# Kernel tuning notes

Hardware: AMD Instinct MI355X
Metric: run time of the kernel (lower is better)

Reference implementation:

```python
import jax, jax.numpy as jnp
import numpy as np

SAMPLE_RATE = 24000.0
HARMONIC_NUM = 8
SINE_AMP = 0.1
DIM = HARMONIC_NUM + 1
BATCH, LENGTH = 16, 480000


def setup_inputs() -> dict:
    key = jax.random.key(0)
    k1, k2, k3 = jax.random.split(key, 3)
    u = jax.random.uniform(k1, (BATCH, LENGTH), dtype=jnp.float32)
    voiced = (jax.random.uniform(k2, (BATCH, LENGTH)) > 0.2).astype(jnp.float32)
    f0 = (80.0 + 400.0 * u) * voiced
    rand_ini = jax.random.uniform(k3, (BATCH, 1, DIM), dtype=jnp.float32)
    return {"f0": f0, "rand_ini": rand_ini}


def reference(f0, rand_ini):
    # f0: [B, L] -> [B, L, 1]
    f0 = f0[..., None]
    harmonics = jnp.arange(1, DIM + 1, dtype=f0.dtype).reshape(1, 1, -1)  # [1,1,DIM]
    rad_values = jnp.mod(f0 * harmonics / SAMPLE_RATE, 1.0)              # [B,L,DIM]
    rad_values = rad_values.at[:, 0:1, :].add(rand_ini)                  # random initial phase
    phase = jnp.cumsum(rad_values, axis=1) * (2.0 * jnp.pi)              # [B,L,DIM]
    uv = (f0 > 0).astype(f0.dtype)                                       # [B,L,1]
    sine_waves = jnp.sin(phase) * SINE_AMP * uv                          # fused scale+mask
    return sine_waves, uv
```

## Files before the change

### kernel.cpp

```cpp
#include <hip/hip_runtime.h>
#include <math.h>

#define BATCH 16
#define LEN 480000
#define NDIM 9
#define CHUNK 4096
#define NCHUNK 118
#define AMP 0.1f

__device__ __forceinline__ float hw_fract(float x) {
#if __has_builtin(__builtin_amdgcn_fractf)
  return __builtin_amdgcn_fractf(x);
#else
  return x - floorf(x);
#endif
}
__device__ __forceinline__ float hw_sin1(float x) {
#if __has_builtin(__builtin_amdgcn_sinf)
  return __builtin_amdgcn_sinf(x);
#else
  return __sinf(x * 6.283185307179586f);
#endif
}

__global__ __launch_bounds__(256) void sg_partial(const float* __restrict__ f0,
                                                  double* __restrict__ part) {
  const int c = blockIdx.x, b = blockIdx.y, t = threadIdx.x;
  const float4* f4 = (const float4*)(f0 + (size_t)b * LEN);
  const int b4 = c * (CHUNK / 4);
  double s = 0.0;
#pragma unroll
  for (int p = 0; p < 4; ++p) {
    int i4 = b4 + p * 256 + t;
    if (i4 < LEN / 4) {
      float4 v = f4[i4];
      s += (double)((v.x + v.y) + (v.z + v.w));
    }
  }
#pragma unroll
  for (int d = 32; d > 0; d >>= 1) s += __shfl_down(s, d, 64);
  __shared__ double ws[4];
  if ((t & 63) == 0) ws[t >> 6] = s;
  __syncthreads();
  if (t == 0) part[b * NCHUNK + c] = (ws[0] + ws[1]) + (ws[2] + ws[3]);
}

__global__ void sg_scan(const double* __restrict__ part, double* __restrict__ off) {
  const int b = threadIdx.x;
  if (b < BATCH) {
    double run = 0.0;
    for (int c = 0; c < NCHUNK; ++c) {
      off[b * NCHUNK + c] = run;
      run += part[b * NCHUNK + c];
    }
  }
}

__global__ __launch_bounds__(256) void sg_main(const float* __restrict__ f0,
                                               const float* __restrict__ rand_ini,
                                               const double* __restrict__ off,
                                               float* __restrict__ out) {
  const int c = blockIdx.x, b = blockIdx.y, t = threadIdx.x;
  const int lane = t & 63, w = t >> 6;

  __shared__ float4 tile[2304];
  __shared__ float wsc[4];

  const float4* f4 = (const float4*)(f0 + (size_t)b * LEN);
  const int base = c * CHUNK;
  const int valid = min(CHUNK, LEN - base);

  float fv[4][4];
  float gs[4];
#pragma unroll
  for (int p = 0; p < 4; ++p) {
    int i4 = base / 4 + p * 256 + t;
    float4 v = make_float4(0.f, 0.f, 0.f, 0.f);
    if (i4 < LEN / 4) v = f4[i4];
    fv[p][0] = v.x; fv[p][1] = v.y; fv[p][2] = v.z; fv[p][3] = v.w;
    gs[p] = (v.x + v.y) + (v.z + v.w);
  }

  float goff[4];
  float running = 0.f;
#pragma unroll
  for (int p = 0; p < 4; ++p) {
    float x = gs[p];
#pragma unroll
    for (int d = 1; d < 64; d <<= 1) {
      float y = __shfl_up(x, d, 64);
      if (lane >= d) x += y;
    }
    if (lane == 63) wsc[w] = x;
    __syncthreads();
    float t0 = wsc[0], t1 = wsc[1], t2 = wsc[2], t3 = wsc[3];
    float tot  = (t0 + t1) + (t2 + t3);
    float wpre = (w > 0 ? t0 : 0.f) + (w > 1 ? t1 : 0.f) + (w > 2 ? t2 : 0.f);
    goff[p] = running + wpre + (x - gs[p]);
    running += tot;
    __syncthreads();
  }

  const double cb = off[b * NCHUNK + c];
  float phi0[NDIM], hsf[NDIM];
#pragma unroll
  for (int h = 0; h < NDIM; ++h) {
    double hs = (double)(h + 1) * (1.0 / 24000.0);
    double p0 = (double)rand_ini[b * NDIM + h] + hs * cb;
    p0 -= floor(p0);
    phi0[h] = (float)p0;
    hsf[h] = (float)hs;
  }

  float4* out4 = (float4*)out;
  const size_t sine4_rowbase = ((size_t)b * LEN * NDIM) / 4;
  const size_t uv4_base = ((size_t)BATCH * LEN * NDIM) / 4 + ((size_t)b * LEN) / 4;

#pragma unroll
  for (int p = 0; p < 4; ++p) {
    const int ebase = base + p * 1024 + 4 * t;
    float P = goff[p];
    float sv[4][NDIM];
    float uvv[4];
#pragma unroll
    for (int e = 0; e < 4; ++e) {
      float f = fv[p][e];
      P += f;
      uvv[e] = (f > 0.f) ? 1.f : 0.f;
      float amp = AMP * uvv[e];
#pragma unroll
      for (int h = 0; h < NDIM; ++h) {
        float ph = hw_fract(phi0[h] + hsf[h] * P);
        sv[e][h] = amp * hw_sin1(ph);
      }
    }
#pragma unroll
    for (int j = 0; j < 9; ++j) {
      const int i0 = 4 * j;
      tile[t * 9 + j] = make_float4(sv[(i0    ) / 9][(i0    ) % 9],
                                    sv[(i0 + 1) / 9][(i0 + 1) % 9],
                                    sv[(i0 + 2) / 9][(i0 + 2) % 9],
                                    sv[(i0 + 3) / 9][(i0 + 3) % 9]);
    }
    if (ebase < LEN)
      out4[uv4_base + (size_t)(base + p * 1024) / 4 + t] =
          make_float4(uvv[0], uvv[1], uvv[2], uvv[3]);
    __syncthreads();
    const int pv = min(max(valid - p * 1024, 0), 1024);
    const int nf4 = (pv * NDIM) >> 2;
    const size_t gb4 = sine4_rowbase + (size_t)(base + p * 1024) * NDIM / 4;
#pragma unroll
    for (int k = 0; k < 9; ++k) {
      int idx = k * 256 + t;
      if (idx < nf4) out4[gb4 + idx] = tile[idx];
    }
    __syncthreads();
  }
}

extern "C" void kernel_launch(void* const* d_in, const int* in_sizes, int n_in,
                              void* d_out, int out_size, void* d_ws, size_t ws_size,
                              hipStream_t stream) {
  const float* f0 = (const float*)d_in[0];
  const float* rand_ini = (const float*)d_in[1];
  float* out = (float*)d_out;

  double* part = (double*)d_ws;
  double* off  = part + (size_t)BATCH * NCHUNK;

  dim3 grid(NCHUNK, BATCH);
  sg_partial<<<grid, 256, 0, stream>>>(f0, part);
  sg_scan<<<1, 64, 0, stream>>>(part, off);
  sg_main<<<grid, 256, 0, stream>>>(f0, rand_ini, off, out);
}
```

Before: 352.2 us.

## Shrink chunks to 1024 and fold the serial scan into the main kernel

```diff
diff --git a/kernel.cpp b/kernel.cpp
--- a/kernel.cpp
+++ b/kernel.cpp
@@ -4,8 +4,8 @@
 #define BATCH 16
 #define LEN 480000
 #define NDIM 9
-#define CHUNK 4096
-#define NCHUNK 118
+#define CHUNK 1024
+#define NCHUNK 469
 #define AMP 0.1f
 
 __device__ __forceinline__ float hw_fract(float x) {
@@ -26,82 +26,60 @@
 __global__ __launch_bounds__(256) void sg_partial(const float* __restrict__ f0,
                                                   double* __restrict__ part) {
   const int c = blockIdx.x, b = blockIdx.y, t = threadIdx.x;
-  const float4* f4 = (const float4*)(f0 + (size_t)b * LEN);
-  const int b4 = c * (CHUNK / 4);
-  double s = 0.0;
-#pragma unroll
-  for (int p = 0; p < 4; ++p) {
-    int i4 = b4 + p * 256 + t;
-    if (i4 < LEN / 4) {
-      float4 v = f4[i4];
-      s += (double)((v.x + v.y) + (v.z + v.w));
-    }
-  }
+  const int i4 = c * 256 + t;
+  float4 v = make_float4(0.f, 0.f, 0.f, 0.f);
+  if (i4 < LEN / 4) v = ((const float4*)(f0 + (size_t)b * LEN))[i4];
+  double s = (double)((v.x + v.y) + (v.z + v.w));
 #pragma unroll
   for (int d = 32; d > 0; d >>= 1) s += __shfl_down(s, d, 64);
   __shared__ double ws[4];
   if ((t & 63) == 0) ws[t >> 6] = s;
   __syncthreads();
-  if (t == 0) part[b * NCHUNK + c] = (ws[0] + ws[1]) + (ws[2] + ws[3]);
-}
-
-__global__ void sg_scan(const double* __restrict__ part, double* __restrict__ off) {
-  const int b = threadIdx.x;
-  if (b < BATCH) {
-    double run = 0.0;
-    for (int c = 0; c < NCHUNK; ++c) {
-      off[b * NCHUNK + c] = run;
-      run += part[b * NCHUNK + c];
-    }
-  }
+  if (t == 0) part[(size_t)b * NCHUNK + c] = (ws[0] + ws[1]) + (ws[2] + ws[3]);
 }
 
 __global__ __launch_bounds__(256) void sg_main(const float* __restrict__ f0,
                                                const float* __restrict__ rand_ini,
-                                               const double* __restrict__ off,
+                                               const double* __restrict__ part,
                                                float* __restrict__ out) {
   const int c = blockIdx.x, b = blockIdx.y, t = threadIdx.x;
   const int lane = t & 63, w = t >> 6;
 
   __shared__ float4 tile[2304];
   __shared__ float wsc[4];
+  __shared__ double dred[4];
+  __shared__ double cbs_s;
 
-  const float4* f4 = (const float4*)(f0 + (size_t)b * LEN);
-  const int base = c * CHUNK;
-  const int valid = min(CHUNK, LEN - base);
+  const int i4 = c * 256 + t;
+  float4 v = make_float4(0.f, 0.f, 0.f, 0.f);
+  if (i4 < LEN / 4) v = ((const float4*)(f0 + (size_t)b * LEN))[i4];
+  const float fvv0 = v.x, fvv1 = v.y, fvv2 = v.z, fvv3 = v.w;
+  const float gs = (v.x + v.y) + (v.z + v.w);
 
-  float fv[4][4];
-  float gs[4];
+  const double* prow = part + (size_t)b * NCHUNK;
+  double s = 0.0;
+  if (t < c) s += prow[t];
+  if (t + 256 < c) s += prow[t + 256];
 #pragma unroll
-  for (int p = 0; p < 4; ++p) {
-    int i4 = base / 4 + p * 256 + t;
-    float4 v = make_float4(0.f, 0.f, 0.f, 0.f);
-    if (i4 < LEN / 4) v = f4[i4];
-    fv[p][0] = v.x; fv[p][1] = v.y; fv[p][2] = v.z; fv[p][3] = v.w;
-    gs[p] = (v.x + v.y) + (v.z + v.w);
+  for (int d = 32; d > 0; d >>= 1) s += __shfl_down(s, d, 64);
+  if (lane == 0) dred[w] = s;
+
+  float x = gs;
+#pragma unroll
+  for (int d = 1; d < 64; d <<= 1) {
+    float y = __shfl_up(x, d, 64);
+    if (lane >= d) x += y;
   }
+  if (lane == 63) wsc[w] = x;
+  __syncthreads();
+  if (t == 0) cbs_s = (dred[0] + dred[1]) + (dred[2] + dred[3]);
+  __syncthreads();
 
-  float goff[4];
-  float running = 0.f;
-#pragma unroll
-  for (int p = 0; p < 4; ++p) {
-    float x = gs[p];
-#pragma unroll
-    for (int d = 1; d < 64; d <<= 1) {
-      float y = __shfl_up(x, d, 64);
-      if (lane >= d) x += y;
-    }
-    if (lane == 63) wsc[w] = x;
-    __syncthreads();
-    float t0 = wsc[0], t1 = wsc[1], t2 = wsc[2], t3 = wsc[3];
-    float tot  = (t0 + t1) + (t2 + t3);
-    float wpre = (w > 0 ? t0 : 0.f) + (w > 1 ? t1 : 0.f) + (w > 2 ? t2 : 0.f);
-    goff[p] = running + wpre + (x - gs[p]);
-    running += tot;
-    __syncthreads();
-  }
+  const float t0 = wsc[0], t1 = wsc[1], t2 = wsc[2];
+  const float wpre = (w > 0 ? t0 : 0.f) + (w > 1 ? t1 : 0.f) + (w > 2 ? t2 : 0.f);
+  float P = wpre + (x - gs);
 
-  const double cb = off[b * NCHUNK + c];
+  const double cb = cbs_s;
   float phi0[NDIM], hsf[NDIM];
 #pragma unroll
   for (int h = 0; h < NDIM; ++h) {
@@ -112,50 +90,43 @@
     hsf[h] = (float)hs;
   }
 
-  float4* out4 = (float4*)out;
-  const size_t sine4_rowbase = ((size_t)b * LEN * NDIM) / 4;
-  const size_t uv4_base = ((size_t)BATCH * LEN * NDIM) / 4 + ((size_t)b * LEN) / 4;
+  float sv[4][NDIM];
+  float uvv[4];
+  const float fvv[4] = {fvv0, fvv1, fvv2, fvv3};
+#pragma unroll
+  for (int e = 0; e < 4; ++e) {
+    const float f = fvv[e];
+    P += f;
+    uvv[e] = (f > 0.f) ? 1.f : 0.f;
+    const float amp = AMP * uvv[e];
+#pragma unroll
+    for (int h = 0; h < NDIM; ++h)
+      sv[e][h] = amp * hw_sin1(hw_fract(phi0[h] + hsf[h] * P));
+  }
 
 #pragma unroll
-  for (int p = 0; p < 4; ++p) {
-    const int ebase = base + p * 1024 + 4 * t;
-    float P = goff[p];
-    float sv[4][NDIM];
-    float uvv[4];
+  for (int j = 0; j < 9; ++j) {
+    const int i0 = 4 * j;
+    tile[t * 9 + j] = make_float4(sv[(i0    ) / 9][(i0    ) % 9],
+                                  sv[(i0 + 1) / 9][(i0 + 1) % 9],
+                                  sv[(i0 + 2) / 9][(i0 + 2) % 9],
+                                  sv[(i0 + 3) / 9][(i0 + 3) % 9]);
+  }
+  __syncthreads();
+
+  float4* out4 = (float4*)out;
+  const int base = c * CHUNK;
+  const int valid = min(CHUNK, LEN - base);
+  const int nf4 = (valid * NDIM) >> 2;
+  const size_t gb4 = ((size_t)b * LEN * NDIM + (size_t)base * NDIM) >> 2;
 #pragma unroll
-    for (int e = 0; e < 4; ++e) {
-      float f = fv[p][e];
-      P += f;
-      uvv[e] = (f > 0.f) ? 1.f : 0.f;
-      float amp = AMP * uvv[e];
-#pragma unroll
-      for (int h = 0; h < NDIM; ++h) {
-        float ph = hw_fract(phi0[h] + hsf[h] * P);
-        sv[e][h] = amp * hw_sin1(ph);
-      }
-    }
-#pragma unroll
-    for (int j = 0; j < 9; ++j) {
-      const int i0 = 4 * j;
-      tile[t * 9 + j] = make_float4(sv[(i0    ) / 9][(i0    ) % 9],
-                                    sv[(i0 + 1) / 9][(i0 + 1) % 9],
-                                    sv[(i0 + 2) / 9][(i0 + 2) % 9],
-                                    sv[(i0 + 3) / 9][(i0 + 3) % 9]);
-    }
-    if (ebase < LEN)
-      out4[uv4_base + (size_t)(base + p * 1024) / 4 + t] =
-          make_float4(uvv[0], uvv[1], uvv[2], uvv[3]);
-    __syncthreads();
-    const int pv = min(max(valid - p * 1024, 0), 1024);
-    const int nf4 = (pv * NDIM) >> 2;
-    const size_t gb4 = sine4_rowbase + (size_t)(base + p * 1024) * NDIM / 4;
-#pragma unroll
-    for (int k = 0; k < 9; ++k) {
-      int idx = k * 256 + t;
-      if (idx < nf4) out4[gb4 + idx] = tile[idx];
-    }
-    __syncthreads();
+  for (int k = 0; k < 9; ++k) {
+    const int idx = k * 256 + t;
+    if (idx < nf4) out4[gb4 + idx] = tile[idx];
   }
+  const size_t uv4_base = ((size_t)BATCH * LEN * NDIM) / 4 + ((size_t)b * LEN) / 4;
+  if (i4 < LEN / 4)
+    out4[uv4_base + i4] = make_float4(uvv[0], uvv[1], uvv[2], uvv[3]);
 }
 
 extern "C" void kernel_launch(void* const* d_in, const int* in_sizes, int n_in,
@@ -166,10 +137,8 @@
   float* out = (float*)d_out;
 
   double* part = (double*)d_ws;
-  double* off  = part + (size_t)BATCH * NCHUNK;
 
   dim3 grid(NCHUNK, BATCH);
   sg_partial<<<grid, 256, 0, stream>>>(f0, part);
-  sg_scan<<<1, 64, 0, stream>>>(part, off);
-  sg_main<<<grid, 256, 0, stream>>>(f0, rand_ini, off, out);
+  sg_main<<<grid, 256, 0, stream>>>(f0, rand_ini, part, out);
 }
```

Measured after the change: 331.6 us. 1.06x faster.
